# Performance work log

Hardware: AMD Instinct MI355X
Metric: run time of the kernel (lower is better)

The kernel has to match this reference:

```python
import jax, jax.numpy as jnp
import numpy as np

B, S, HID, H = 2, 2048, 1024, 16
D = HID // H
LAMBDA_INIT = 0.8
GN_EPS = 1e-5


def setup_inputs() -> dict:
    rng = jax.random.key(0)
    ks = jax.random.split(rng, 12)
    w = 0.02
    return {
        "query": jax.random.normal(ks[0], (B, S, HID), dtype=jnp.float32),
        "key": jax.random.normal(ks[1], (B, S, HID), dtype=jnp.float32),
        "value": jax.random.normal(ks[2], (B, S, HID), dtype=jnp.float32),
        "attention_mask": jnp.ones((B, S), dtype=jnp.float32),
        # params ([in, out] layout; x @ W)
        "Wq": jax.random.normal(ks[3], (HID, H * D * 2), dtype=jnp.float32) * w,
        "Wk": jax.random.normal(ks[4], (HID, H * D * 2), dtype=jnp.float32) * w,
        "Wv": jax.random.normal(ks[5], (HID, H * D), dtype=jnp.float32) * w,
        "Wo": jax.random.normal(ks[6], (H * D, HID), dtype=jnp.float32) * w,
        "lam_q1": jax.random.normal(ks[7], (D,), dtype=jnp.float32),
        "lam_q2": jax.random.normal(ks[8], (D,), dtype=jnp.float32),
        "lam_k1": jax.random.normal(ks[9], (D,), dtype=jnp.float32),
        "lam_k2": jax.random.normal(ks[10], (D,), dtype=jnp.float32),
        "gn_weight": jnp.ones((H * D,), dtype=jnp.float32),
        "gn_bias": jnp.zeros((H * D,), dtype=jnp.float32),
    }


def reference(query, key, value, attention_mask, Wq, Wk, Wv, Wo,
              lam_q1, lam_q2, lam_k1, lam_k2, gn_weight, gn_bias):
    b, s, hid = query.shape
    h, d = H, hid // H
    rs = 1.0 / jnp.sqrt(jnp.asarray(d, query.dtype))

    q = (query @ Wq).reshape(b, s, h, 2 * d).transpose(0, 2, 1, 3)   # [b,h,s,2d]
    k = (key @ Wk).reshape(b, s, h, 2 * d).transpose(0, 2, 1, 3)
    v = (value @ Wv).reshape(b, s, h, d).transpose(0, 2, 1, 3)       # [b,h,s,d]

    Q1, Q2 = q[..., :d], q[..., d:]
    K1, K2 = k[..., :d], k[..., d:]
    s1 = jnp.einsum('bhqd,bhkd->bhqk', Q1, K1) * rs
    s2 = jnp.einsum('bhqd,bhkd->bhqk', Q2, K2) * rs

    # ALiBi bias: slopes[h] * (pos_q - pos_k), subtracted from scores
    pos = jnp.arange(s, dtype=query.dtype)
    slopes = 2.0 ** (-8.0 * jnp.arange(1, h + 1, dtype=query.dtype) / h)
    alibi = slopes[None, :, None, None] * (pos[:, None] - pos[None, :])[None, None]
    causal = jnp.triu(jnp.full((s, s), -1e9, dtype=query.dtype), k=1)[None, None]
    pad = (1.0 - attention_mask)[:, None, None, :] * -1e9
    add = -alibi + causal + pad

    w1 = jax.nn.softmax(s1 + add, axis=-1)
    w2 = jax.nn.softmax(s2 + add, axis=-1)

    lam = (jnp.exp(jnp.dot(lam_q1, lam_k1))
           - jnp.exp(jnp.dot(lam_q2, lam_k2)) + LAMBDA_INIT)
    dw = w1 - lam * w2

    attn = jnp.einsum('bhqk,bhkd->bhqd', dw, v).transpose(0, 2, 1, 3)  # [b,s,h,d]

    # GroupNorm(groups=h, channels=h*d) over [b, C, L]: per (b, head) normalize over (seq, d)
    mean = attn.mean(axis=(1, 3), keepdims=True)
    var = ((attn - mean) ** 2).mean(axis=(1, 3), keepdims=True)
    normed = (attn - mean) / jnp.sqrt(var + GN_EPS)
    normed = normed * gn_weight.reshape(1, 1, h, d) + gn_bias.reshape(1, 1, h, d)

    out = normed * (1.0 - LAMBDA_INIT)
    return out.reshape(b, s, h * d) @ Wo
```

## Files before the change

### kernel.cpp

```cpp
#include <hip/hip_runtime.h>
#include <cstdint>
#include <cstddef>

#define SQ 2048
#define NH 16
#define DH 64
#define HIDN 1024

typedef __attribute__((ext_vector_type(8))) short bf16x8;
typedef __attribute__((ext_vector_type(4))) float f32x4;
typedef __attribute__((ext_vector_type(2))) unsigned u32x2;

__device__ inline short f2b(float x) {
  union { float f; unsigned u; } un; un.f = x;
  unsigned r = un.u + 0x7fffu + ((un.u >> 16) & 1u);
  return (short)(r >> 16);
}

__device__ inline unsigned cvt_pk(float lo, float hi) {
  unsigned r;
  asm("v_cvt_pk_bf16_f32 %0, %1, %2" : "=v"(r) : "v"(lo), "v"(hi));
  return r;
}

__device__ inline f32x4 mfma16(u32x2 a, u32x2 b, f32x4 c) {
  asm("v_mfma_f32_16x16x16_bf16 %0, %1, %2, %0" : "+v"(c) : "v"(a), "v"(b));
  return c;
}

__device__ inline void gl_lds16(const void* g, void* l) {
  __builtin_amdgcn_global_load_lds(
      (const __attribute__((address_space(1))) void*)g,
      (__attribute__((address_space(3))) void*)l, 16, 0, 0);
}

__global__ __launch_bounds__(256) void qkv_to_bf16(const float4* __restrict__ q,
                                                   const float4* __restrict__ k,
                                                   const float4* __restrict__ v,
                                                   short4* __restrict__ out) {
  int i = blockIdx.x * 256 + threadIdx.x;
  const float4* src = (i < 1048576) ? q : ((i < 2097152) ? k : v);
  float4 val = src[i & 1048575];
  short4 o;
  o.x = f2b(val.x); o.y = f2b(val.y); o.z = f2b(val.z); o.w = f2b(val.w);
  out[i] = o;
}

__global__ __launch_bounds__(256) void wconv4(const float* __restrict__ Wq,
                                              const float* __restrict__ Wk,
                                              const float* __restrict__ Wv,
                                              const float* __restrict__ Wo,
                                              short* __restrict__ WqT, short* __restrict__ WkT,
                                              short* __restrict__ WvT, short* __restrict__ WoT) {
  __shared__ float t[32][33];
  int z = blockIdx.z;
  int N = (z < 2) ? 2048 : 1024;
  if (blockIdx.x * 32 >= N) return;
  const float* W = (z == 0) ? Wq : (z == 1) ? Wk : (z == 2) ? Wv : Wo;
  short* Wt = (z == 0) ? WqT : (z == 1) ? WkT : (z == 2) ? WvT : WoT;
  const int K = 1024;
  int n0 = blockIdx.x * 32, k0 = blockIdx.y * 32;
  int tx = threadIdx.x & 31, ty = threadIdx.x >> 5;
#pragma unroll
  for (int r = 0; r < 4; ++r)
    t[ty + r * 8][tx] = W[(size_t)(k0 + ty + r * 8) * N + n0 + tx];
  __syncthreads();
#pragma unroll
  for (int r = 0; r < 4; ++r)
    Wt[(size_t)(n0 + ty + r * 8) * K + k0 + tx] = f2b(t[tx][ty + r * 8]);
}

__global__ void lam_k(const float* __restrict__ q1, const float* __restrict__ q2,
                      const float* __restrict__ k1, const float* __restrict__ k2,
                      float* __restrict__ out) {
  int i = threadIdx.x;
  float d1 = q1[i] * k1[i], d2 = q2[i] * k2[i];
#pragma unroll
  for (int x = 1; x < 64; x <<= 1) { d1 += __shfl_xor(d1, x); d2 += __shfl_xor(d2, x); }
  if (i == 0) out[0] = __expf(d1) - __expf(d2) + 0.8f;
}

__global__ __launch_bounds__(256) void padk(const float* __restrict__ mask,
                                            float* __restrict__ padl2) {
  int i = blockIdx.x * 256 + threadIdx.x;
  padl2[i] = (1.0f - mask[i]) * (-1.0e9f) * 1.44269504089f;
}

#define STG(dst, srcp, kt, kk)                                                        \
  {                                                                                   \
    gl_lds16(srcp + (size_t)r0_ * 1024 + ((kt) << 6) + ((kk) << 5) + c0_,             \
             &dst[ch0_ << 3]);                                                        \
    gl_lds16(srcp + (size_t)r1_ * 1024 + ((kt) << 6) + ((kk) << 5) + c1_,             \
             &dst[ch1_ << 3]);                                                        \
  }

__global__ __launch_bounds__(256) void proj3(const short* __restrict__ Abase,
                                             const short* __restrict__ Btbase,
                                             short* __restrict__ QKout,
                                             short* __restrict__ Vtb) {
  __shared__ __align__(16) short As[2][2][128 * 32];
  __shared__ __align__(16) short Bs[2][2][128 * 32];
  const int bid = blockIdx.x;
  const int wk = (bid & 7) * 160 + (bid >> 3);
  int z, my, nx;
  if (wk < 1024) { z = wk >> 9; int r = wk & 511; my = r >> 4; nx = r & 15; }
  else { z = 2; int r = wk - 1024; my = r >> 3; nx = r & 7; }

  const int tid = threadIdx.x;
  const int lane = tid & 63, w = tid >> 6;
  const int l15 = lane & 15, lhi = lane >> 4;
  const int wr = w >> 1, wc = w & 1;
  const int m0 = my * 128, n0 = nx * 128;

  const short* Ag = Abase + (size_t)z * 4194304 + (size_t)m0 * 1024;
  const short* Bg = Btbase + (size_t)z * 2097152 + (size_t)n0 * 1024;

  const int ch0_ = tid, ch1_ = tid + 256;
  const int r0_ = ch0_ >> 2, c0_ = (ch0_ & 3) << 3;
  const int r1_ = ch1_ >> 2, c1_ = (ch1_ & 3) << 3;

  f32x4 acc[4][4];
#pragma unroll
  for (int i = 0; i < 4; ++i)
#pragma unroll
    for (int j = 0; j < 4; ++j) acc[i][j] = (f32x4){0.f, 0.f, 0.f, 0.f};

  STG(As[0][0], Ag, 0, 0); STG(Bs[0][0], Bg, 0, 0);
  STG(As[0][1], Ag, 0, 1); STG(Bs[0][1], Bg, 0, 1);
  asm volatile("s_waitcnt vmcnt(4)" ::: "memory");
  __builtin_amdgcn_s_barrier();

  for (int kt = 0; kt < 16; ++kt) {
    const int buf = kt & 1;
#pragma unroll
    for (int kk = 0; kk < 2; ++kk) {
      const short* Ah = As[buf][kk];
      const short* Bh = Bs[buf][kk];
      bf16x8 af[4], bfr[4];
#pragma unroll
      for (int mi = 0; mi < 4; ++mi)
        af[mi] = *(const bf16x8*)&Ah[((wr * 64 + mi * 16 + l15) << 5) + (lhi << 3)];
#pragma unroll
      for (int ni = 0; ni < 4; ++ni)
        bfr[ni] = *(const bf16x8*)&Bh[((wc * 64 + ni * 16 + l15) << 5) + (lhi << 3)];
      if (kt < 15) {
        STG(As[buf ^ 1][kk], Ag, kt + 1, kk);
        STG(Bs[buf ^ 1][kk], Bg, kt + 1, kk);
      }
      __builtin_amdgcn_s_barrier();
      __builtin_amdgcn_s_setprio(1);
#pragma unroll
      for (int mi = 0; mi < 4; ++mi)
#pragma unroll
        for (int ni = 0; ni < 4; ++ni)
          acc[mi][ni] = __builtin_amdgcn_mfma_f32_16x16x32_bf16(af[mi], bfr[ni], acc[mi][ni], 0, 0, 0);
      __builtin_amdgcn_s_setprio(0);
      if (kt < 15) asm volatile("s_waitcnt vmcnt(4)" ::: "memory");
      else         asm volatile("s_waitcnt vmcnt(0)" ::: "memory");
      __builtin_amdgcn_s_barrier();
    }
  }

#pragma unroll
  for (int mi = 0; mi < 4; ++mi) {
#pragma unroll
    for (int ni = 0; ni < 4; ++ni) {
#pragma unroll
      for (int j = 0; j < 4; ++j) {
        int m = m0 + wr * 64 + mi * 16 + (lhi << 2) + j;
        int n = n0 + wc * 64 + ni * 16 + l15;
        float v = acc[mi][ni][j];
        int s = m & (SQ - 1), bb = m >> 11;
        if (z < 2) {
          int h = n >> 7, t = n & 127, path = t >> 6, tt = t & 63;
          (QKout + (size_t)z * 8388608)
              [((((size_t)(bb * NH + h) * 2 + path) * SQ + s) << 6) + tt] = f2b(v);
        } else {
          int h = n >> 6, t = n & 63;
          Vtb[(((size_t)(bb * NH + h) << 6) + t) * SQ + s] = f2b(v);
        }
      }
    }
  }
}

__global__ __launch_bounds__(256) void gemm_out(const short* __restrict__ A,
                                                const short* __restrict__ Bt,
                                                float* __restrict__ Cout) {
  __shared__ __align__(16) short As[2][2][128 * 32];
  __shared__ __align__(16) short Bs[2][2][128 * 32];
  const int bid = blockIdx.x;
  const int wk = (bid & 7) * 32 + (bid >> 3);
  const int my = wk >> 3, nx = wk & 7;

  const int tid = threadIdx.x;
  const int lane = tid & 63, w = tid >> 6;
  const int l15 = lane & 15, lhi = lane >> 4;
  const int wr = w >> 1, wc = w & 1;
  const int m0 = my * 128, n0 = nx * 128;

  const short* Ag = A + (size_t)m0 * 1024;
  const short* Bg = Bt + (size_t)n0 * 1024;

  const int ch0_ = tid, ch1_ = tid + 256;
  const int r0_ = ch0_ >> 2, c0_ = (ch0_ & 3) << 3;
  const int r1_ = ch1_ >> 2, c1_ = (ch1_ & 3) << 3;

  f32x4 acc[4][4];
#pragma unroll
  for (int i = 0; i < 4; ++i)
#pragma unroll
    for (int j = 0; j < 4; ++j) acc[i][j] = (f32x4){0.f, 0.f, 0.f, 0.f};

  STG(As[0][0], Ag, 0, 0); STG(Bs[0][0], Bg, 0, 0);
  STG(As[0][1], Ag, 0, 1); STG(Bs[0][1], Bg, 0, 1);
  asm volatile("s_waitcnt vmcnt(4)" ::: "memory");
  __builtin_amdgcn_s_barrier();

  for (int kt = 0; kt < 16; ++kt) {
    const int buf = kt & 1;
#pragma unroll
    for (int kk = 0; kk < 2; ++kk) {
      const short* Ah = As[buf][kk];
      const short* Bh = Bs[buf][kk];
      bf16x8 af[4], bfr[4];
#pragma unroll
      for (int mi = 0; mi < 4; ++mi)
        af[mi] = *(const bf16x8*)&Ah[((wr * 64 + mi * 16 + l15) << 5) + (lhi << 3)];
#pragma unroll
      for (int ni = 0; ni < 4; ++ni)
        bfr[ni] = *(const bf16x8*)&Bh[((wc * 64 + ni * 16 + l15) << 5) + (lhi << 3)];
      if (kt < 15) {
        STG(As[buf ^ 1][kk], Ag, kt + 1, kk);
        STG(Bs[buf ^ 1][kk], Bg, kt + 1, kk);
      }
      __builtin_amdgcn_s_barrier();
      __builtin_amdgcn_s_setprio(1);
#pragma unroll
      for (int mi = 0; mi < 4; ++mi)
#pragma unroll
        for (int ni = 0; ni < 4; ++ni)
          acc[mi][ni] = __builtin_amdgcn_mfma_f32_16x16x32_bf16(af[mi], bfr[ni], acc[mi][ni], 0, 0, 0);
      __builtin_amdgcn_s_setprio(0);
      if (kt < 15) asm volatile("s_waitcnt vmcnt(4)" ::: "memory");
      else         asm volatile("s_waitcnt vmcnt(0)" ::: "memory");
      __builtin_amdgcn_s_barrier();
    }
  }

#pragma unroll
  for (int mi = 0; mi < 4; ++mi)
#pragma unroll
    for (int ni = 0; ni < 4; ++ni)
#pragma unroll
      for (int j = 0; j < 4; ++j) {
        int m = m0 + wr * 64 + mi * 16 + (lhi << 2) + j;
        int n = n0 + wc * 64 + ni * 16 + l15;
        Cout[(size_t)m * 1024 + n] = acc[mi][ni][j];
      }
}

__global__ __launch_bounds__(256) void diff_attn(
    const short* __restrict__ Qp, const short* __restrict__ Kp,
    const short* __restrict__ Vt, const float* __restrict__ padl2,
    const float* __restrict__ lamp, float* __restrict__ attn,
    float* __restrict__ part) {
  __shared__ __align__(16) short K1s[2][64 * 64];
  __shared__ __align__(16) short K2s[2][64 * 64];
  __shared__ __align__(16) short Vts[2][64 * 64];
  __shared__ float red[8];

  const int bid = blockIdx.x;
  const int rk = bid >> 5, bh = bid & 31;
  const int qtA = 31 - rk, qtB = rk;
  const int ntA = qtA + 1, ntT = ntA + qtB + 1;
  const int b = bh >> 4, h = bh & 15;
  const int tid = threadIdx.x, lane = tid & 63, w = tid >> 6;
  const int l15 = lane & 15, lhi = lane >> 4;
  const int sw7 = l15 & 7;
  const int u0 = (lhi ^ sw7) << 3, u1 = ((4 + lhi) ^ sw7) << 3;

  const float L2E = 1.44269504089f;
  const float slope = exp2f(-0.5f * (float)(h + 1));
  const float SC = 0.125f * L2E;
  const float sl2 = slope * L2E;

  f32x4 ck[4];
#pragma unroll
  for (int cf = 0; cf < 4; ++cf)
#pragma unroll
    for (int j = 0; j < 4; ++j)
      ck[cf][j] = sl2 * (float)(16 * cf + 4 * lhi + j);

  const short* Q1g = Qp + (((size_t)bh * 2 + 0) * SQ) * DH;
  const short* Q2g = Qp + (((size_t)bh * 2 + 1) * SQ) * DH;
  const short* K1g = Kp + (((size_t)bh * 2 + 0) * SQ) * DH;
  const short* K2g = Kp + (((size_t)bh * 2 + 1) * SQ) * DH;
  const short* Vtg = Vt + (size_t)bh * DH * SQ;
  const float* padb = padl2 + (b << 11);

  int ucf[4];
#pragma unroll
  for (int cf = 0; cf < 4; ++cf)
    ucf[cf] = (((2 * cf + (lhi >> 1)) ^ sw7) << 1) + (lhi & 1);

  const int sidx0 = tid, sidx1 = 256 + tid;
  const int srow0 = sidx0 >> 3, sus0 = ((sidx0 & 7) ^ (srow0 & 7)) << 3;
  const int srow1 = sidx1 >> 3, sus1 = ((sidx1 & 7) ^ (srow1 & 7)) << 3;

#define STAGE(buf, k0s)                                                          \
  {                                                                              \
    gl_lds16(K1g + (size_t)((k0s) + srow0) * DH + sus0, &K1s[buf][sidx0 << 3]);  \
    gl_lds16(K2g + (size_t)((k0s) + srow0) * DH + sus0, &K2s[buf][sidx0 << 3]);  \
    gl_lds16(Vtg + (size_t)srow0 * SQ + (k0s) + sus0, &Vts[buf][sidx0 << 3]);    \
    gl_lds16(K1g + (size_t)((k0s) + srow1) * DH + sus1, &K1s[buf][sidx1 << 3]);  \
    gl_lds16(K2g + (size_t)((k0s) + srow1) * DH + sus1, &K2s[buf][sidx1 << 3]);  \
    gl_lds16(Vtg + (size_t)srow1 * SQ + (k0s) + sus1, &Vts[buf][sidx1 << 3]);    \
  }

  int cur = 0;
  int itg = 0;
  STAGE(0, 0);
  asm volatile("s_waitcnt vmcnt(0)" ::: "memory");
  __builtin_amdgcn_s_barrier();

  const float lamv = lamp[0];

  for (int ph = 0; ph < 2; ++ph) {
    const int qt = ph ? qtB : qtA;
    const int nt = qt + 1;
    const int wq0 = qt * 64 + (w << 4);
    const int q = wq0 + l15;
    const float qb8 = sl2 * (float)q + 8.0f;

    bf16x8 aq[2][2];
#pragma unroll
    for (int kk = 0; kk < 2; ++kk) {
      aq[0][kk] = *(const bf16x8*)&Q1g[(size_t)q * DH + kk * 32 + lhi * 8];
      aq[1][kk] = *(const bf16x8*)&Q2g[(size_t)q * DH + kk * 32 + lhi * 8];
    }
    f32x4 cq[4];
#pragma unroll
    for (int cf = 0; cf < 4; ++cf)
#pragma unroll
      for (int j = 0; j < 4; ++j) cq[cf][j] = ck[cf][j] - qb8;

    f32x4 acc[2][4];
    float ll[2] = {0.f, 0.f};
#pragma unroll
    for (int p = 0; p < 2; ++p)
#pragma unroll
      for (int i = 0; i < 4; ++i) acc[p][i] = (f32x4){0.f, 0.f, 0.f, 0.f};

    for (int kt = 0; kt < nt; ++kt, ++itg) {
      const int k0 = kt << 6;
      int g = itg + 1;
      if (g < ntT) {
        int k0n = ((g < ntA) ? g : g - ntA) << 6;
        STAGE(cur ^ 1, k0n);
      }

      const float t0 = sl2 * (float)k0;
      f32x4 base4[4];
#pragma unroll
      for (int cf = 0; cf < 4; ++cf) {
        f32x4 p4 = *(const f32x4*)&padb[k0 + 16 * cf + 4 * lhi];
#pragma unroll
        for (int j = 0; j < 4; ++j) base4[cf][j] = cq[cf][j] + (t0 + p4[j]);
      }
      const bool diag = (kt == nt - 1);

      u32x2 pa[2][4];
#pragma unroll
      for (int p = 0; p < 2; ++p) {
        const short* Ks = (p == 0) ? K1s[cur] : K2s[cur];
        f32x4 sv[4];
#pragma unroll
        for (int cf = 0; cf < 4; ++cf) {
          int rb = (cf * 16 + l15) << 6;
          f32x4 z = (f32x4){0.f, 0.f, 0.f, 0.f};
          bf16x8 ka = *(const bf16x8*)&Ks[rb + u0];
          bf16x8 kb = *(const bf16x8*)&Ks[rb + u1];
          sv[cf] = __builtin_amdgcn_mfma_f32_16x16x32_bf16(ka, aq[p][0], z, 0, 0, 0);
          sv[cf] = __builtin_amdgcn_mfma_f32_16x16x32_bf16(kb, aq[p][1], sv[cf], 0, 0, 0);
        }
        float rsum = 0.f;
#pragma unroll
        for (int cf = 0; cf < 4; ++cf) {
          float pv[4];
#pragma unroll
          for (int j = 0; j < 4; ++j) pv[j] = sv[cf][j] * SC + base4[cf][j];
          if (diag) {
#pragma unroll
            for (int j = 0; j < 4; ++j) {
              int kc = k0 + 16 * cf + 4 * lhi + j;
              pv[j] = (kc > q) ? -1.0e9f : pv[j];
            }
          }
          float e0 = exp2f(pv[0]);
          float e1 = exp2f(pv[1]);
          float e2 = exp2f(pv[2]);
          float e3 = exp2f(pv[3]);
          rsum += (e0 + e1) + (e2 + e3);
          pa[p][cf][0] = cvt_pk(e0, e1);
          pa[p][cf][1] = cvt_pk(e2, e3);
        }
        ll[p] += rsum;
      }

#pragma unroll
      for (int df = 0; df < 4; ++df) {
        const u32x2* vrow = (const u32x2*)&Vts[cur][(df * 16 + l15) << 6];
#pragma unroll
        for (int cf = 0; cf < 4; ++cf) {
          u32x2 vb = vrow[ucf[cf]];
          acc[0][df] = mfma16(pa[0][cf], vb, acc[0][df]);
          acc[1][df] = mfma16(pa[1][cf], vb, acc[1][df]);
        }
      }

      asm volatile("s_waitcnt vmcnt(0)" ::: "memory");
      __builtin_amdgcn_s_barrier();
      cur ^= 1;
    }

#pragma unroll
    for (int p = 0; p < 2; ++p) {
      ll[p] += __shfl_xor(ll[p], 16);
      ll[p] += __shfl_xor(ll[p], 32);
    }
    float li1 = 1.0f / ll[0], li2 = lamv / ll[1];
    float li1b[4], li2b[4];
#pragma unroll
    for (int j = 0; j < 4; ++j) {
      li1b[j] = __shfl(li1, (lhi << 2) + j);
      li2b[j] = __shfl(li2, (lhi << 2) + j);
    }
    float lsum = 0.f, lsq = 0.f;
#pragma unroll
    for (int df = 0; df < 4; ++df)
#pragma unroll
      for (int j = 0; j < 4; ++j) {
        int qq = wq0 + (lhi << 2) + j;
        float o = acc[0][df][j] * li1b[j] - acc[1][df][j] * li2b[j];
        attn[((size_t)b * SQ + qq) * HIDN + (h << 6) + (df << 4) + l15] = o;
        lsum += o; lsq += o * o;
      }
#pragma unroll
    for (int x = 1; x < 64; x <<= 1) {
      lsum += __shfl_xor(lsum, x);
      lsq += __shfl_xor(lsq, x);
    }
    if (lane == 0) { red[w] = lsum; red[4 + w] = lsq; }
    __syncthreads();
    if (tid == 0) {
      part[((size_t)bh * 32 + qt) * 2] = red[0] + red[1] + red[2] + red[3];
      part[((size_t)bh * 32 + qt) * 2 + 1] = red[4] + red[5] + red[6] + red[7];
    }
  }
#undef STAGE
}

__global__ void stats_fin(const float* __restrict__ part, float* __restrict__ mi) {
  int t = threadIdx.x;
  int bh = t >> 5, i = t & 31;
  float s = part[(bh * 32 + i) * 2];
  float ss = part[(bh * 32 + i) * 2 + 1];
#pragma unroll
  for (int x = 1; x < 32; x <<= 1) { s += __shfl_xor(s, x); ss += __shfl_xor(ss, x); }
  if (i == 0) {
    float n = (float)(SQ * DH);
    float mean = s / n;
    float var = ss / n - mean * mean;
    mi[bh * 2] = mean;
    mi[bh * 2 + 1] = rsqrtf(var + 1e-5f);
  }
}

__global__ __launch_bounds__(256) void gn_apply(const float* __restrict__ attn,
                                                const float* __restrict__ mi,
                                                const float* __restrict__ gnw,
                                                const float* __restrict__ gnb,
                                                short* __restrict__ X) {
  size_t i = (size_t)blockIdx.x * 256 + threadIdx.x;
  size_t base = i << 2;
  int r = (int)(base >> 10);
  int c = (int)(base & 1023);
  int bh = ((r >> 11) << 4) + (c >> 6);
  float mean = mi[bh * 2], inv = mi[bh * 2 + 1];
  float4 a = *(const float4*)&attn[base];
  short4 o;
  o.x = f2b(((a.x - mean) * inv * gnw[c + 0] + gnb[c + 0]) * 0.2f);
  o.y = f2b(((a.y - mean) * inv * gnw[c + 1] + gnb[c + 1]) * 0.2f);
  o.z = f2b(((a.z - mean) * inv * gnw[c + 2] + gnb[c + 2]) * 0.2f);
  o.w = f2b(((a.w - mean) * inv * gnw[c + 3] + gnb[c + 3]) * 0.2f);
  *(short4*)&X[base] = o;
}

extern "C" void kernel_launch(void* const* d_in, const int* in_sizes, int n_in,
                              void* d_out, int out_size, void* d_ws, size_t ws_size,
                              hipStream_t stream) {
  const float* query = (const float*)d_in[0];
  const float* key = (const float*)d_in[1];
  const float* value = (const float*)d_in[2];
  const float* mask = (const float*)d_in[3];
  const float* Wq = (const float*)d_in[4];
  const float* Wk = (const float*)d_in[5];
  const float* Wv = (const float*)d_in[6];
  const float* Wo = (const float*)d_in[7];
  const float* lq1 = (const float*)d_in[8];
  const float* lq2 = (const float*)d_in[9];
  const float* lk1 = (const float*)d_in[10];
  const float* lk2 = (const float*)d_in[11];
  const float* gnw = (const float*)d_in[12];
  const float* gnb = (const float*)d_in[13];

  char* ws = (char*)d_ws;
  short* WqT = (short*)(ws + 0);
  short* WkT = (short*)(ws + 4194304);
  short* WvT = (short*)(ws + 8388608);
  short* WoT = (short*)(ws + 10485760);
  short* qb = (short*)(ws + 12582912);
  short* Qp = (short*)(ws + 37748736);
  short* Kp = (short*)(ws + 54525952);
  short* Vtb = (short*)(ws + 71303168);
  float* attn = (float*)(ws + 12582912);
  short* X = (short*)(ws + 29360128);
  float* part = (float*)(ws + 79691776);
  float* mi = (float*)(ws + 79708160);
  float* lam = (float*)(ws + 79708416);
  float* padl2 = (float*)(ws + 79708672);

  qkv_to_bf16<<<12288, 256, 0, stream>>>((const float4*)query, (const float4*)key,
                                         (const float4*)value, (short4*)qb);
  wconv4<<<dim3(64, 32, 4), 256, 0, stream>>>(Wq, Wk, Wv, Wo, WqT, WkT, WvT, WoT);
  lam_k<<<1, 64, 0, stream>>>(lq1, lq2, lk1, lk2, lam);
  padk<<<16, 256, 0, stream>>>(mask, padl2);

  proj3<<<dim3(1280), 256, 0, stream>>>(qb, WqT, Qp, Vtb);

  diff_attn<<<dim3(512), 256, 0, stream>>>(Qp, Kp, Vtb, padl2, lam, attn, part);
  stats_fin<<<1, 1024, 0, stream>>>(part, mi);
  gn_apply<<<4096, 256, 0, stream>>>(attn, mi, gnw, gnb, X);
  gemm_out<<<dim3(256), 256, 0, stream>>>(X, WoT, (float*)d_out);
}
```

Measured before the change: 206.7 us.

## Split differential attention's two softmax branches across separate waves in 512-thread blocks

The attention kernel now launches 512 threads per block. Waves 0-3 compute the Q1/K1 softmax branch and waves 4-7 compute the Q2/K2 branch, where before each wave computed both. The second branch's scaled output goes through a new 16KB LDS buffer and is subtracted by the first group before the store and the statistics step. This halves per-wave register pressure and doubles the waves available to hide latency. In exchange it costs more LDS, an extra barrier per q-tile, and LDS round trips for the combine.

Measured after the change: 239.3 us. +15.8%, slower.

```diff
diff --git a/kernel.cpp b/kernel.cpp
--- a/kernel.cpp
+++ b/kernel.cpp
@@ -260,7 +260,7 @@
       }
 }
 
-__global__ __launch_bounds__(256) void diff_attn(
+__global__ __launch_bounds__(512) void diff_attn(
     const short* __restrict__ Qp, const short* __restrict__ Kp,
     const short* __restrict__ Vt, const float* __restrict__ padl2,
     const float* __restrict__ lamp, float* __restrict__ attn,
@@ -268,14 +268,18 @@
   __shared__ __align__(16) short K1s[2][64 * 64];
   __shared__ __align__(16) short K2s[2][64 * 64];
   __shared__ __align__(16) short Vts[2][64 * 64];
+  __shared__ float xbuf[64 * 64];
   __shared__ float red[8];
 
   const int bid = blockIdx.x;
   const int rk = bid >> 5, bh = bid & 31;
   const int qtA = 31 - rk, qtB = rk;
-  const int ntA = qtA + 1, ntT = ntA + qtB + 1;
+  const int ntA = qtA + 1;
+  const int ntT = 33;
   const int b = bh >> 4, h = bh & 15;
   const int tid = threadIdx.x, lane = tid & 63, w = tid >> 6;
+  const int rg = w & 3;
+  const int p = w >> 2;
   const int l15 = lane & 15, lhi = lane >> 4;
   const int sw7 = l15 & 7;
   const int u0 = (lhi ^ sw7) << 3, u1 = ((4 + lhi) ^ sw7) << 3;
@@ -292,8 +296,7 @@
     for (int j = 0; j < 4; ++j)
       ck[cf][j] = sl2 * (float)(16 * cf + 4 * lhi + j);
 
-  const short* Q1g = Qp + (((size_t)bh * 2 + 0) * SQ) * DH;
-  const short* Q2g = Qp + (((size_t)bh * 2 + 1) * SQ) * DH;
+  const short* Qg = Qp + (((size_t)bh * 2 + p) * SQ) * DH;
   const short* K1g = Kp + (((size_t)bh * 2 + 0) * SQ) * DH;
   const short* K2g = Kp + (((size_t)bh * 2 + 1) * SQ) * DH;
   const short* Vtg = Vt + (size_t)bh * DH * SQ;
@@ -304,61 +307,48 @@
   for (int cf = 0; cf < 4; ++cf)
     ucf[cf] = (((2 * cf + (lhi >> 1)) ^ sw7) << 1) + (lhi & 1);
 
-  const int sidx0 = tid, sidx1 = 256 + tid;
-  const int srow0 = sidx0 >> 3, sus0 = ((sidx0 & 7) ^ (srow0 & 7)) << 3;
-  const int srow1 = sidx1 >> 3, sus1 = ((sidx1 & 7) ^ (srow1 & 7)) << 3;
-
-#define STAGE(buf, k0s)                                                          \
-  {                                                                              \
-    gl_lds16(K1g + (size_t)((k0s) + srow0) * DH + sus0, &K1s[buf][sidx0 << 3]);  \
-    gl_lds16(K2g + (size_t)((k0s) + srow0) * DH + sus0, &K2s[buf][sidx0 << 3]);  \
-    gl_lds16(Vtg + (size_t)srow0 * SQ + (k0s) + sus0, &Vts[buf][sidx0 << 3]);    \
-    gl_lds16(K1g + (size_t)((k0s) + srow1) * DH + sus1, &K1s[buf][sidx1 << 3]);  \
-    gl_lds16(K2g + (size_t)((k0s) + srow1) * DH + sus1, &K2s[buf][sidx1 << 3]);  \
-    gl_lds16(Vtg + (size_t)srow1 * SQ + (k0s) + sus1, &Vts[buf][sidx1 << 3]);    \
-  }
-
-  int cur = 0;
-  int itg = 0;
+  const int srow = tid >> 3, sus = ((tid & 7) ^ (srow & 7)) << 3;
+
+#define STAGE(bf, k0s)                                                        \
+  {                                                                           \
+    gl_lds16(K1g + (size_t)((k0s) + srow) * DH + sus, &K1s[bf][tid << 3]);    \
+    gl_lds16(K2g + (size_t)((k0s) + srow) * DH + sus, &K2s[bf][tid << 3]);    \
+    gl_lds16(Vtg + (size_t)srow * SQ + (k0s) + sus, &Vts[bf][tid << 3]);      \
+  }
+#define K0OF(g) ((((g) < ntA) ? (g) : (g)-ntA) << 6)
+
   STAGE(0, 0);
   asm volatile("s_waitcnt vmcnt(0)" ::: "memory");
   __builtin_amdgcn_s_barrier();
 
   const float lamv = lamp[0];
+  int itg = 0, buf = 0;
 
   for (int ph = 0; ph < 2; ++ph) {
     const int qt = ph ? qtB : qtA;
     const int nt = qt + 1;
-    const int wq0 = qt * 64 + (w << 4);
+    const int wq0 = qt * 64 + (rg << 4);
     const int q = wq0 + l15;
     const float qb8 = sl2 * (float)q + 8.0f;
 
-    bf16x8 aq[2][2];
-#pragma unroll
-    for (int kk = 0; kk < 2; ++kk) {
-      aq[0][kk] = *(const bf16x8*)&Q1g[(size_t)q * DH + kk * 32 + lhi * 8];
-      aq[1][kk] = *(const bf16x8*)&Q2g[(size_t)q * DH + kk * 32 + lhi * 8];
-    }
+    bf16x8 aq[2];
+#pragma unroll
+    for (int kk = 0; kk < 2; ++kk)
+      aq[kk] = *(const bf16x8*)&Qg[(size_t)q * DH + kk * 32 + lhi * 8];
     f32x4 cq[4];
 #pragma unroll
     for (int cf = 0; cf < 4; ++cf)
 #pragma unroll
       for (int j = 0; j < 4; ++j) cq[cf][j] = ck[cf][j] - qb8;
 
-    f32x4 acc[2][4];
-    float ll[2] = {0.f, 0.f};
-#pragma unroll
-    for (int p = 0; p < 2; ++p)
-#pragma unroll
-      for (int i = 0; i < 4; ++i) acc[p][i] = (f32x4){0.f, 0.f, 0.f, 0.f};
+    f32x4 acc[4];
+    float ll = 0.f;
+#pragma unroll
+    for (int i = 0; i < 4; ++i) acc[i] = (f32x4){0.f, 0.f, 0.f, 0.f};
 
     for (int kt = 0; kt < nt; ++kt, ++itg) {
       const int k0 = kt << 6;
-      int g = itg + 1;
-      if (g < ntT) {
-        int k0n = ((g < ntA) ? g : g - ntA) << 6;
-        STAGE(cur ^ 1, k0n);
-      }
+      if (itg + 1 < ntT) STAGE(buf ^ 1, K0OF(itg + 1));
 
       const float t0 = sl2 * (float)k0;
       f32x4 base4[4];
@@ -370,95 +360,98 @@
       }
       const bool diag = (kt == nt - 1);
 
-      u32x2 pa[2][4];
-#pragma unroll
-      for (int p = 0; p < 2; ++p) {
-        const short* Ks = (p == 0) ? K1s[cur] : K2s[cur];
-        f32x4 sv[4];
-#pragma unroll
-        for (int cf = 0; cf < 4; ++cf) {
-          int rb = (cf * 16 + l15) << 6;
-          f32x4 z = (f32x4){0.f, 0.f, 0.f, 0.f};
-          bf16x8 ka = *(const bf16x8*)&Ks[rb + u0];
-          bf16x8 kb = *(const bf16x8*)&Ks[rb + u1];
-          sv[cf] = __builtin_amdgcn_mfma_f32_16x16x32_bf16(ka, aq[p][0], z, 0, 0, 0);
-          sv[cf] = __builtin_amdgcn_mfma_f32_16x16x32_bf16(kb, aq[p][1], sv[cf], 0, 0, 0);
+      const short* Ks = p ? K2s[buf] : K1s[buf];
+      f32x4 sv[4];
+#pragma unroll
+      for (int cf = 0; cf < 4; ++cf) {
+        int rb = (cf * 16 + l15) << 6;
+        f32x4 z = (f32x4){0.f, 0.f, 0.f, 0.f};
+        bf16x8 ka = *(const bf16x8*)&Ks[rb + u0];
+        bf16x8 kb = *(const bf16x8*)&Ks[rb + u1];
+        sv[cf] = __builtin_amdgcn_mfma_f32_16x16x32_bf16(ka, aq[0], z, 0, 0, 0);
+        sv[cf] = __builtin_amdgcn_mfma_f32_16x16x32_bf16(kb, aq[1], sv[cf], 0, 0, 0);
+      }
+      u32x2 pa[4];
+      float rsum = 0.f;
+#pragma unroll
+      for (int cf = 0; cf < 4; ++cf) {
+        float pv[4];
+#pragma unroll
+        for (int j = 0; j < 4; ++j) pv[j] = sv[cf][j] * SC + base4[cf][j];
+        if (diag) {
+#pragma unroll
+          for (int j = 0; j < 4; ++j) {
+            int kc = k0 + 16 * cf + 4 * lhi + j;
+            pv[j] = (kc > q) ? -1.0e9f : pv[j];
+          }
         }
-        float rsum = 0.f;
-#pragma unroll
-        for (int cf = 0; cf < 4; ++cf) {
-          float pv[4];
-#pragma unroll
-          for (int j = 0; j < 4; ++j) pv[j] = sv[cf][j] * SC + base4[cf][j];
-          if (diag) {
-#pragma unroll
-            for (int j = 0; j < 4; ++j) {
-              int kc = k0 + 16 * cf + 4 * lhi + j;
-              pv[j] = (kc > q) ? -1.0e9f : pv[j];
-            }
-          }
-          float e0 = exp2f(pv[0]);
-          float e1 = exp2f(pv[1]);
-          float e2 = exp2f(pv[2]);
-          float e3 = exp2f(pv[3]);
-          rsum += (e0 + e1) + (e2 + e3);
-          pa[p][cf][0] = cvt_pk(e0, e1);
-          pa[p][cf][1] = cvt_pk(e2, e3);
-        }
-        ll[p] += rsum;
-      }
+        float e0 = exp2f(pv[0]);
+        float e1 = exp2f(pv[1]);
+        float e2 = exp2f(pv[2]);
+        float e3 = exp2f(pv[3]);
+        rsum += (e0 + e1) + (e2 + e3);
+        pa[cf][0] = cvt_pk(e0, e1);
+        pa[cf][1] = cvt_pk(e2, e3);
+      }
+      ll += rsum;
 
 #pragma unroll
       for (int df = 0; df < 4; ++df) {
-        const u32x2* vrow = (const u32x2*)&Vts[cur][(df * 16 + l15) << 6];
-#pragma unroll
-        for (int cf = 0; cf < 4; ++cf) {
-          u32x2 vb = vrow[ucf[cf]];
-          acc[0][df] = mfma16(pa[0][cf], vb, acc[0][df]);
-          acc[1][df] = mfma16(pa[1][cf], vb, acc[1][df]);
-        }
+        const u32x2* vrow = (const u32x2*)&Vts[buf][(df * 16 + l15) << 6];
+#pragma unroll
+        for (int cf = 0; cf < 4; ++cf)
+          acc[df] = mfma16(pa[cf], vrow[ucf[cf]], acc[df]);
       }
 
       asm volatile("s_waitcnt vmcnt(0)" ::: "memory");
       __builtin_amdgcn_s_barrier();
-      cur ^= 1;
-    }
-
-#pragma unroll
-    for (int p = 0; p < 2; ++p) {
-      ll[p] += __shfl_xor(ll[p], 16);
-      ll[p] += __shfl_xor(ll[p], 32);
-    }
-    float li1 = 1.0f / ll[0], li2 = lamv / ll[1];
-    float li1b[4], li2b[4];
-#pragma unroll
-    for (int j = 0; j < 4; ++j) {
-      li1b[j] = __shfl(li1, (lhi << 2) + j);
-      li2b[j] = __shfl(li2, (lhi << 2) + j);
-    }
-    float lsum = 0.f, lsq = 0.f;
-#pragma unroll
-    for (int df = 0; df < 4; ++df)
-#pragma unroll
-      for (int j = 0; j < 4; ++j) {
-        int qq = wq0 + (lhi << 2) + j;
-        float o = acc[0][df][j] * li1b[j] - acc[1][df][j] * li2b[j];
-        attn[((size_t)b * SQ + qq) * HIDN + (h << 6) + (df << 4) + l15] = o;
-        lsum += o; lsq += o * o;
-      }
-#pragma unroll
-    for (int x = 1; x < 64; x <<= 1) {
-      lsum += __shfl_xor(lsum, x);
-      lsq += __shfl_xor(lsq, x);
-    }
-    if (lane == 0) { red[w] = lsum; red[4 + w] = lsq; }
+      buf ^= 1;
+    }
+
+    ll += __shfl_xor(ll, 16);
+    ll += __shfl_xor(ll, 32);
+    float li = (p ? lamv : 1.0f) / ll;
+    float lib[4];
+#pragma unroll
+    for (int j = 0; j < 4; ++j) lib[j] = __shfl(li, (lhi << 2) + j);
+
+    if (p == 1) {
+#pragma unroll
+      for (int df = 0; df < 4; ++df)
+#pragma unroll
+        for (int j = 0; j < 4; ++j)
+          xbuf[(size_t)((rg << 4) + (lhi << 2) + j) * 64 + (df << 4) + l15] =
+              acc[df][j] * lib[j];
+    }
+    __syncthreads();
+    if (p == 0) {
+      float lsum = 0.f, lsq = 0.f;
+#pragma unroll
+      for (int df = 0; df < 4; ++df)
+#pragma unroll
+        for (int j = 0; j < 4; ++j) {
+          int qq = wq0 + (lhi << 2) + j;
+          float o = acc[df][j] * lib[j] -
+                    xbuf[(size_t)((rg << 4) + (lhi << 2) + j) * 64 + (df << 4) + l15];
+          attn[((size_t)b * SQ + qq) * HIDN + (h << 6) + (df << 4) + l15] = o;
+          lsum += o; lsq += o * o;
+        }
+#pragma unroll
+      for (int x = 1; x < 64; x <<= 1) {
+        lsum += __shfl_xor(lsum, x);
+        lsq += __shfl_xor(lsq, x);
+      }
+      if (lane == 0) { red[rg] = lsum; red[4 + rg] = lsq; }
+    }
     __syncthreads();
     if (tid == 0) {
       part[((size_t)bh * 32 + qt) * 2] = red[0] + red[1] + red[2] + red[3];
       part[((size_t)bh * 32 + qt) * 2 + 1] = red[4] + red[5] + red[6] + red[7];
     }
+    __syncthreads();
   }
 #undef STAGE
+#undef K0OF
 }
 
 __global__ void stats_fin(const float* __restrict__ part, float* __restrict__ mi) {
@@ -539,7 +532,7 @@
 
   proj3<<<dim3(1280), 256, 0, stream>>>(qb, WqT, Qp, Vtb);
 
-  diff_attn<<<dim3(512), 256, 0, stream>>>(Qp, Kp, Vtb, padl2, lam, attn, part);
+  diff_attn<<<dim3(512), 512, 0, stream>>>(Qp, Kp, Vtb, padl2, lam, attn, part);
   stats_fin<<<1, 1024, 0, stream>>>(part, mi);
   gn_apply<<<4096, 256, 0, stream>>>(attn, mi, gnw, gnb, X);
   gemm_out<<<dim3(256), 256, 0, stream>>>(X, WoT, (float*)d_out);
```
